# Kernel optimization log

Hardware: AMD Instinct MI355X
Metric: run time of the kernel (lower is better)

## Reference

```python
import jax, jax.numpy as jnp
import numpy as np
from jax import lax

# SLAYER neuron / simulation constants (netParams)
THETA = 1.0      # spike threshold
TAU_SR = 4.0     # PSP (SRM) kernel time constant
TAU_REF = 1.0    # refractory kernel time constant
SCALE_REF = 2.0  # refractory scale (kernel amplitude = -scaleRef*theta)
TAU_RHO = 1.0    # surrogate-gradient width (used in bwd only)
SCALE_RHO = 1.0

B, F_IN, T = 8, 6300, 500  # 6300 = 50*63*2
HID, OUT = 32, 20


def _alpha_scan(x, d):
    """Causal conv with alpha kernel k*d**k along last (time) axis via 2-state recurrence.
    x: [..., T]. y[t] = sum_{j<=t} x[j]*(t-j)*d**(t-j)."""
    xt = jnp.moveaxis(x, -1, 0)  # [T, ...]
    zero = jnp.zeros_like(xt[0])

    def step(carry, xi):
        z, y = carry
        y_new = d * (y + z)       # y[t] = d*(y[t-1] + z[t-1])
        z_new = d * z + xi        # z[t] = d*z[t-1] + x[t]
        return (z_new, y_new), y_new

    _, ys = lax.scan(step, (zero, zero), xt)
    return jnp.moveaxis(ys, 0, -1)


def psp(x):
    """SLAYER psp: convolve spike train with SRM kernel eps(k) = (k/tauSr)*exp(1-k/tauSr)."""
    d = float(np.exp(-1.0 / TAU_SR))
    return jnp.float32(np.e / TAU_SR) * _alpha_scan(x, d)


def _spike_impl(p):
    """Iterative threshold + refractory. p: [..., T] membrane input (post-psp, post-dense).
    Refractory kernel: ref(k) = -scaleRef*theta*(k/tauRef)*exp(1-k/tauRef), realized by the
    same 2-state alpha recurrence driven by emitted spikes."""
    d = float(np.exp(-1.0 / TAU_REF))
    C = jnp.float32(-SCALE_REF * THETA * np.e / TAU_REF)
    pt = jnp.moveaxis(p, -1, 0)  # [T, ...]
    zero = jnp.zeros_like(pt[0])

    def step(carry, pi):
        z, y = carry
        y_new = d * (y + z)                 # alpha state from past spikes (lag>=1)
        u = pi + C * y_new                  # membrane potential incl. refractory
        s = (u >= THETA).astype(pi.dtype)   # hard threshold
        z_new = d * z + s
        return (z_new, y_new), s

    _, ss = lax.scan(step, (zero, zero), pt)
    return jnp.moveaxis(ss, 0, -1)


def spike(p):
    return _spike_impl(p)


def setup_inputs() -> dict:
    key = jax.random.key(0)
    k1, k2, k3 = jax.random.split(key, 3)
    downsampled = (jax.random.uniform(k1, (B, F_IN, T)) < 0.05).astype(jnp.float32)
    w1 = jax.random.normal(k2, (HID, F_IN), jnp.float32) * 0.05
    w2 = jax.random.normal(k3, (OUT, HID), jnp.float32) * 0.3
    return {"downsampled": downsampled, "w1": w1, "w2": w2}


def reference(downsampled, w1, w2):
    # spike_1 = spike(psp(downsampled))
    s1 = spike(psp(downsampled))
    # spike_2 = spike(fc1(psp(spike_1)))
    s2 = spike(jnp.einsum('of,bft->bot', w1, psp(s1)))
    # spike_3 = spike(fc2(psp(spike_2)))
    s3 = spike(jnp.einsum('of,bft->bot', w2, psp(s2)))
    return s3
```

## Files before the change

kernel.cpp:

```cpp
#include <hip/hip_runtime.h>
#include <stdint.h>

#define NB 8
#define F_IN 6300
#define NT 500
#define HID 32
#define NOUT 20
#define NW 99

#define D_SR   0.7788007830714049f
#define S_SR   0.6795704571147613f
#define D_REF  0.36787944117144233f
#define C_REF  -5.43656365691809f

__global__ __launch_bounds__(256) void k0_transpose(const float* __restrict__ w1,
                                                    float* __restrict__ w1t) {
  __shared__ float tl[64][33];
  const int f0 = blockIdx.x * 64;
  const int tid = threadIdx.x;
  const int r = tid & 63, g = tid >> 6;
#pragma unroll
  for (int oo = 0; oo < 32; oo += 4) {
    int o = oo + g;
    int f = f0 + r;
    tl[r][o] = (f < F_IN) ? w1[o * F_IN + f] : 0.f;
  }
  __syncthreads();
#pragma unroll
  for (int k = 0; k < 8; k++) {
    int idx = k * 256 + tid;
    int rr = idx >> 5, cc = idx & 31;
    int f = f0 + rr;
    if (f < F_IN) w1t[(size_t)f * 32 + cc] = tl[rr][cc];
  }
}

#define CH_T 100

__global__ __launch_bounds__(64, 1) void k1_layer1(const float* __restrict__ x,
                                                   uint64_t* __restrict__ masks) {
  __shared__ __align__(16) float tileT[64][104];
  const int wi = blockIdx.x;
  const int b  = blockIdx.y;
  const int lane = threadIdx.x;
  const int f = wi * 64 + lane;
  const uint64_t vmask = __ballot(f < F_IN);
  const float* xblk = x + (size_t)b * F_IN * NT;
  uint64_t* mrow = masks + ((size_t)b * NW + wi) * NT;

  int goff[25], doff[25];
#pragma unroll
  for (int k = 0; k < 25; k++) {
    int idx = k * 64 + lane;
    int fid = idx / 25;
    int j = idx - fid * 25;
    int rf = wi * 64 + fid;
    if (rf >= F_IN) rf = F_IN - 1;
    goff[k] = rf * NT + 4 * j;
    doff[k] = fid * 104 + 4 * j;
  }

  float z1 = 0.f, y1 = 0.f, zr = 0.f, yr = 0.f;
  float* tbase = &tileT[0][0];

#pragma unroll 1
  for (int c = 0; c < 5; c++) {
    const float* gb = xblk + c * CH_T;
    float4 ld[25];
#pragma unroll
    for (int k = 0; k < 25; k++) ld[k] = *(const float4*)(gb + goff[k]);
#pragma unroll
    for (int k = 0; k < 25; k++) *(float4*)(tbase + doff[k]) = ld[k];

    const float4* lrow = (const float4*)&tileT[lane][0];
    float4 rbuf[4];
#pragma unroll
    for (int i = 0; i < 4; i++) rbuf[i] = lrow[i];
    uint64_t keep0 = 0, keep1 = 0;
#pragma unroll
    for (int g = 0; g < 25; g++) {
      float4 xq = rbuf[g & 3];
      if (g + 4 < 25) rbuf[g & 3] = lrow[g + 4];
      float xs[4] = {xq.x, xq.y, xq.z, xq.w};
#pragma unroll
      for (int e = 0; e < 4; e++) {
        const int tc = g * 4 + e;
        float xi = xs[e];
        y1 = __fmul_rn(D_SR, __fadd_rn(y1, z1));
        z1 = __fadd_rn(__fmul_rn(D_SR, z1), xi);
        float p = __fmul_rn(S_SR, y1);
        yr = __fmul_rn(D_REF, __fadd_rn(yr, zr));
        float u = __fadd_rn(p, __fmul_rn(C_REF, yr));
        bool s = (u >= 1.0f);
        zr = __fadd_rn(__fmul_rn(D_REF, zr), s ? 1.0f : 0.0f);
        uint64_t m = __ballot(s);
        if (tc < 64) { if (lane == tc)      keep0 = m; }
        else         { if (lane == tc - 64) keep1 = m; }
      }
    }
    uint64_t* mp = mrow + c * CH_T;
    mp[lane] = keep0 & vmask;
    if (lane < CH_T - 64) mp[64 + lane] = keep1 & vmask;
  }
}

__global__ __launch_bounds__(512) void k2_fc1(const float* __restrict__ w1t,
                                              const uint64_t* __restrict__ masks,
                                              double* __restrict__ R) {
  __shared__ double part[8][32];
  const int tid = threadIdx.x;
  const int wv = tid >> 6;
  const int lane = tid & 63;
  const int half = lane >> 5;
  const int o = lane & 31;
  const int b = blockIdx.x;
  const int t = blockIdx.y * 4 + (wv & 3);
  const int seg = wv >> 2;
  const int wbeg = seg * 50, wend = seg ? NW : 50;
  const uint64_t* mbase = masks + (size_t)b * NW * NT + t;
  const char* wrow = (const char*)w1t + o * 4;
  double acc0 = 0.0, acc1 = 0.0, acc2 = 0.0, acc3 = 0.0;

  int wi = wbeg + half;
  uint64_t mcur = (wi < wend) ? mbase[(size_t)wi * NT] : 0;
  for (; wi < wend; wi += 2) {
    uint64_t mnext = (wi + 2 < wend) ? mbase[(size_t)(wi + 2) * NT] : 0;
    const uint32_t base0 = ((uint32_t)wi << 13);
    uint32_t w = (uint32_t)mcur;
    uint32_t boff = base0;
#pragma unroll
    for (int sub = 0; sub < 2; sub++) {
      while (w) {
        uint32_t i0 = __builtin_ctz(w);                 uint32_t w1_ = w & (w - 1);
        uint32_t i1 = w1_ ? __builtin_ctz(w1_) : 0u;    uint32_t w2_ = w1_ ? (w1_ & (w1_ - 1)) : 0u;
        uint32_t i2 = w2_ ? __builtin_ctz(w2_) : 0u;    uint32_t w3_ = w2_ ? (w2_ & (w2_ - 1)) : 0u;
        uint32_t i3 = w3_ ? __builtin_ctz(w3_) : 0u;    w = w3_ ? (w3_ & (w3_ - 1)) : 0u;
        float a0 = *(const float*)(wrow + boff + (i0 << 7));
        float a1 = *(const float*)(wrow + boff + (i1 << 7));
        float a2 = *(const float*)(wrow + boff + (i2 << 7));
        float a3 = *(const float*)(wrow + boff + (i3 << 7));
        a1 = w1_ ? a1 : 0.0f;
        a2 = w2_ ? a2 : 0.0f;
        a3 = w3_ ? a3 : 0.0f;
        acc0 += (double)a0;
        acc1 += (double)a1;
        acc2 += (double)a2;
        acc3 += (double)a3;
      }
      w = (uint32_t)(mcur >> 32);
      boff = base0 + (32u << 7);
    }
    mcur = mnext;
  }
  double acc = (acc0 + acc1) + (acc2 + acc3);
  int hi2 = __shfl_xor(__double2hiint(acc), 32);
  int lo2 = __shfl_xor(__double2loint(acc), 32);
  acc += __hiloint2double(hi2, lo2);
  if (half == 0) part[wv][o] = acc;
  __syncthreads();
  if (wv < 4 && half == 0) {
    double tot = part[wv][o] + part[wv + 4][o];
    R[((size_t)b * HID + o) * NT + t] = tot;
  }
}

#define SNN_FAST_STEP(rin, EMIT)                                                \
  {                                                                             \
    y2 = __builtin_fma(dsr, y2, w);                                   \
    z2 = __builtin_fma(dsr, z2, (rin));                               \
    w  = dsr * z2;                                                              \
    double p  = ssr * y2;                                                       \
    double u0 = __builtin_fma(cr, q, p);                                        \
    double u1 = u0 + K;                                                         \
    double u  = sp ? u1 : u0;                                                   \
    bool s = (u >= 1.0);                                                        \
    double yr = q + (sp ? dre : 0.0);                                 \
    double zr = zrd + (sp ? 1.0 : 0.0);                           \
    zrd = dre * zr;                                                             \
    q = __builtin_fma(dre, yr, dre * zrd);                             \
    sp = s;                                                                     \
    EMIT                                                                        \
  }

__global__ __launch_bounds__(64) void k3_spike2(const double* __restrict__ R,
                                                uint32_t* __restrict__ s2m) {
  const int blk = blockIdx.x;
  const int lane = threadIdx.x;
  const int half = lane >> 5;
  const int b = blk * 2 + half;
  const int h = lane & 31;
  const double2* r2 = (const double2*)(R + ((size_t)b * HID + h) * NT);
  uint32_t* m0 = s2m + (size_t)(blk * 2) * NT;
  uint32_t* m1 = s2m + (size_t)(blk * 2 + 1) * NT;

  const double dsr = (double)D_SR, ssr = (double)S_SR;
  const double dre = (double)D_REF, cr = (double)C_REF;
  const double K = cr * dre;
  double y2 = 0, z2 = 0, w = 0, q = 0, zrd = 0;
  bool sp = false;

  double2 bufa[8], bufb[8];
#pragma unroll
  for (int i = 0; i < 8; i++) { bufa[i] = r2[i * 2]; bufb[i] = r2[i * 2 + 1]; }

  for (int g8 = 0; g8 < 16; g8++) {
#pragma unroll
    for (int j = 0; j < 8; j++) {
      const int g = g8 * 8 + j;
      if (g >= 125) break;
      const int t = g * 4;
      double2 va = bufa[j], vb = bufb[j];
      SNN_FAST_STEP(va.x, { uint64_t m = __ballot(s);
        if (lane == 0) { m0[t] = (uint32_t)m; m1[t] = (uint32_t)(m >> 32); } })
      SNN_FAST_STEP(va.y, { uint64_t m = __ballot(s);
        if (lane == 0) { m0[t + 1] = (uint32_t)m; m1[t + 1] = (uint32_t)(m >> 32); } })
      SNN_FAST_STEP(vb.x, { uint64_t m = __ballot(s);
        if (lane == 0) { m0[t + 2] = (uint32_t)m; m1[t + 2] = (uint32_t)(m >> 32); } })
      SNN_FAST_STEP(vb.y, { uint64_t m = __ballot(s);
        if (lane == 0) { m0[t + 3] = (uint32_t)m; m1[t + 3] = (uint32_t)(m >> 32); } })
      if (g + 8 < 125) { bufa[j] = r2[(g + 8) * 2]; bufb[j] = r2[(g + 8) * 2 + 1]; }
    }
  }
}

__global__ __launch_bounds__(256) void k4_fc2(const float* __restrict__ w2,
                                              const uint32_t* __restrict__ s2m,
                                              double* __restrict__ R3) {
  __shared__ float w2l[NOUT * HID];
  const int tid = threadIdx.x;
  for (int i = tid; i < NOUT * HID; i += 256) w2l[i] = w2[i];
  __syncthreads();
  int id = blockIdx.x * 256 + tid;
  if (id >= NB * NOUT * NT) return;
  int t = id % NT;
  int bo = id / NT;
  int o = bo % NOUT;
  int b = bo / NOUT;
  uint32_t m = s2m[(size_t)b * NT + t];
  const float* wr = w2l + o * HID;
  double acc = 0.0;
  while (m) {
    uint32_t i0 = __builtin_ctz(m);                 uint32_t m1_ = m & (m - 1);
    uint32_t i1 = m1_ ? __builtin_ctz(m1_) : 0u;    uint32_t m2_ = m1_ ? (m1_ & (m1_ - 1)) : 0u;
    uint32_t i2 = m2_ ? __builtin_ctz(m2_) : 0u;    uint32_t m3_ = m2_ ? (m2_ & (m2_ - 1)) : 0u;
    uint32_t i3 = m3_ ? __builtin_ctz(m3_) : 0u;    m = m3_ ? (m3_ & (m3_ - 1)) : 0u;
    float a0 = wr[i0];
    float a1 = m1_ ? wr[i1] : 0.0f;
    float a2 = m2_ ? wr[i2] : 0.0f;
    float a3 = m3_ ? wr[i3] : 0.0f;
    acc += (double)a0;
    acc += (double)a1;
    acc += (double)a2;
    acc += (double)a3;
  }
  R3[id] = acc;
}

__global__ __launch_bounds__(64) void k5_out(const double* __restrict__ R3,
                                             float* __restrict__ out) {
  int id = blockIdx.x * 64 + threadIdx.x;
  if (id >= NB * NOUT) return;
  const double2* r2 = (const double2*)(R3 + (size_t)id * NT);
  float* orow = out + (size_t)id * NT;

  const double dsr = (double)D_SR, ssr = (double)S_SR;
  const double dre = (double)D_REF, cr = (double)C_REF;
  const double K = cr * dre;
  double y2 = 0, z2 = 0, w = 0, q = 0, zrd = 0;
  bool sp = false;

  double2 bufa[8], bufb[8];
#pragma unroll
  for (int i = 0; i < 8; i++) { bufa[i] = r2[i * 2]; bufb[i] = r2[i * 2 + 1]; }

  for (int g8 = 0; g8 < 16; g8++) {
#pragma unroll
    for (int j = 0; j < 8; j++) {
      const int g = g8 * 8 + j;
      if (g >= 125) break;
      double2 va = bufa[j], vb = bufb[j];
      float4 ov;
      SNN_FAST_STEP(va.x, { ov.x = s ? 1.0f : 0.0f; })
      SNN_FAST_STEP(va.y, { ov.y = s ? 1.0f : 0.0f; })
      SNN_FAST_STEP(vb.x, { ov.z = s ? 1.0f : 0.0f; })
      SNN_FAST_STEP(vb.y, { ov.w = s ? 1.0f : 0.0f; })
      *(float4*)(orow + g * 4) = ov;
      if (g + 8 < 125) { bufa[j] = r2[(g + 8) * 2]; bufb[j] = r2[(g + 8) * 2 + 1]; }
    }
  }
}

extern "C" void kernel_launch(void* const* d_in, const int* in_sizes, int n_in,
                              void* d_out, int out_size, void* d_ws, size_t ws_size,
                              hipStream_t stream) {
  const float* x  = (const float*)d_in[0];
  const float* w1 = (const float*)d_in[1];
  const float* w2 = (const float*)d_in[2];
  float* out = (float*)d_out;

  uint8_t* ws = (uint8_t*)d_ws;
  const size_t W1T_BYTES  = (size_t)F_IN * HID * 4;
  const size_t MASK_BYTES = (size_t)NB * NW * NT * 8;
  const size_t R_BYTES    = (size_t)NB * HID * NT * 8;
  const size_t S2M_BYTES  = (size_t)NB * NT * 4;
  float*    w1t   = (float*)ws;
  uint64_t* masks = (uint64_t*)(ws + W1T_BYTES);
  double*   R     = (double*)(ws + W1T_BYTES + MASK_BYTES);
  uint32_t* s2m   = (uint32_t*)(ws + W1T_BYTES + MASK_BYTES + R_BYTES);
  double*   R3    = (double*)(ws + W1T_BYTES + MASK_BYTES + R_BYTES + S2M_BYTES);

  k0_transpose<<<99, 256, 0, stream>>>(w1, w1t);
  k1_layer1<<<dim3(NW, NB), 64, 0, stream>>>(x, masks);
  k2_fc1<<<dim3(NB, NT / 4), 512, 0, stream>>>(w1t, masks, R);
  k3_spike2<<<4, 64, 0, stream>>>(R, s2m);
  k4_fc2<<<(NB * NOUT * NT + 255) / 256, 256, 0, stream>>>(w2, s2m, R3);
  k5_out<<<3, 64, 0, stream>>>(R3, out);
}
```

Baseline: 283.6 us.

## Pre-pack input spike trains into bitmasks in a wide parallel kernel

Adds a highly parallel pre-pass, merged with the weight transpose into one launch, that reads the float input spike trains and ballots them into 64-bit time masks per feature row. The layer-1 recurrence kernel then reads only eight words per feature instead of staging float tiles through shared memory. The goal is to move the bulk input read out of the low-occupancy serial scan kernel into a bandwidth-friendly kernel. The packing assumes inputs are exactly binary (it tests >0.5), and it adds a workspace buffer and one extra write and read of the packed data.

```diff
diff --git a/kernel.cpp b/kernel.cpp
--- a/kernel.cpp
+++ b/kernel.cpp
@@ -7,17 +7,41 @@
 #define HID 32
 #define NOUT 20
 #define NW 99
+#define NWD 8
 
 #define D_SR   0.7788007830714049f
 #define S_SR   0.6795704571147613f
 #define D_REF  0.36787944117144233f
 #define C_REF  -5.43656365691809f
 
-__global__ __launch_bounds__(256) void k0_transpose(const float* __restrict__ w1,
-                                                    float* __restrict__ w1t) {
+#define NROWB ((NB * F_IN) / 4)
+
+__global__ __launch_bounds__(256) void k0_pack(const float* __restrict__ x,
+                                               const float* __restrict__ w1,
+                                               uint64_t* __restrict__ xb,
+                                               float* __restrict__ w1t) {
+  const int bid = blockIdx.x;
+  const int tid = threadIdx.x;
+  if (bid < NROWB) {
+    const int row = bid * 4 + (tid >> 6);
+    const int lane = tid & 63;
+    const float* xr = x + (size_t)row * NT;
+    uint64_t m[8];
+#pragma unroll
+    for (int k = 0; k < 8; k++) {
+      int t = k * 64 + lane;
+      float v = (t < NT) ? xr[t] : 0.f;
+      m[k] = __ballot(v > 0.5f);
+    }
+    if (lane == 0) {
+      uint64_t* dst = xb + (size_t)row * NWD;
+#pragma unroll
+      for (int k = 0; k < 8; k++) dst[k] = m[k];
+    }
+    return;
+  }
   __shared__ float tl[64][33];
-  const int f0 = blockIdx.x * 64;
-  const int tid = threadIdx.x;
+  const int f0 = (bid - NROWB) * 64;
   const int r = tid & 63, g = tid >> 6;
 #pragma unroll
   for (int oo = 0; oo < 32; oo += 4) {
@@ -35,72 +59,47 @@
   }
 }
 
-#define CH_T 100
-
-__global__ __launch_bounds__(64, 1) void k1_layer1(const float* __restrict__ x,
+__global__ __launch_bounds__(64, 1) void k1_layer1(const uint64_t* __restrict__ xb,
                                                    uint64_t* __restrict__ masks) {
-  __shared__ __align__(16) float tileT[64][104];
   const int wi = blockIdx.x;
   const int b  = blockIdx.y;
   const int lane = threadIdx.x;
   const int f = wi * 64 + lane;
   const uint64_t vmask = __ballot(f < F_IN);
-  const float* xblk = x + (size_t)b * F_IN * NT;
+  const int fc = (f < F_IN) ? f : (F_IN - 1);
+  const uint64_t* xr = xb + ((size_t)b * F_IN + fc) * NWD;
   uint64_t* mrow = masks + ((size_t)b * NW + wi) * NT;
 
-  int goff[25], doff[25];
-#pragma unroll
-  for (int k = 0; k < 25; k++) {
-    int idx = k * 64 + lane;
-    int fid = idx / 25;
-    int j = idx - fid * 25;
-    int rf = wi * 64 + fid;
-    if (rf >= F_IN) rf = F_IN - 1;
-    goff[k] = rf * NT + 4 * j;
-    doff[k] = fid * 104 + 4 * j;
-  }
-
-  float z1 = 0.f, y1 = 0.f, zr = 0.f, yr = 0.f;
-  float* tbase = &tileT[0][0];
+  float y1 = 0.f, z1 = 0.f, yr = 0.f, zr = 0.f;
+  uint64_t wcur = xr[0];
 
 #pragma unroll 1
-  for (int c = 0; c < 5; c++) {
-    const float* gb = xblk + c * CH_T;
-    float4 ld[25];
-#pragma unroll
-    for (int k = 0; k < 25; k++) ld[k] = *(const float4*)(gb + goff[k]);
-#pragma unroll
-    for (int k = 0; k < 25; k++) *(float4*)(tbase + doff[k]) = ld[k];
-
-    const float4* lrow = (const float4*)&tileT[lane][0];
-    float4 rbuf[4];
-#pragma unroll
-    for (int i = 0; i < 4; i++) rbuf[i] = lrow[i];
-    uint64_t keep0 = 0, keep1 = 0;
-#pragma unroll
-    for (int g = 0; g < 25; g++) {
-      float4 xq = rbuf[g & 3];
-      if (g + 4 < 25) rbuf[g & 3] = lrow[g + 4];
-      float xs[4] = {xq.x, xq.y, xq.z, xq.w};
-#pragma unroll
-      for (int e = 0; e < 4; e++) {
-        const int tc = g * 4 + e;
-        float xi = xs[e];
-        y1 = __fmul_rn(D_SR, __fadd_rn(y1, z1));
-        z1 = __fadd_rn(__fmul_rn(D_SR, z1), xi);
-        float p = __fmul_rn(S_SR, y1);
-        yr = __fmul_rn(D_REF, __fadd_rn(yr, zr));
-        float u = __fadd_rn(p, __fmul_rn(C_REF, yr));
-        bool s = (u >= 1.0f);
-        zr = __fadd_rn(__fmul_rn(D_REF, zr), s ? 1.0f : 0.0f);
-        uint64_t m = __ballot(s);
-        if (tc < 64) { if (lane == tc)      keep0 = m; }
-        else         { if (lane == tc - 64) keep1 = m; }
-      }
-    }
-    uint64_t* mp = mrow + c * CH_T;
-    mp[lane] = keep0 & vmask;
-    if (lane < CH_T - 64) mp[64 + lane] = keep1 & vmask;
+  for (int gg = 0; gg < 8; gg++) {
+    const int gn = (gg < 7) ? gg + 1 : 7;
+    uint64_t wnxt = xr[gn];
+    const uint32_t wlo = (uint32_t)wcur;
+    const uint32_t whi = (uint32_t)(wcur >> 32);
+    uint64_t keep = 0;
+#pragma unroll
+    for (int j = 0; j < 64; j++) {
+      const uint32_t bw = (j < 32) ? wlo : whi;
+      const bool xbit = ((bw >> (j & 31)) & 1u) != 0u;
+      float zm = __fmul_rn(D_SR, z1);
+      y1 = __fmul_rn(D_SR, __fadd_rn(y1, z1));
+      z1 = xbit ? __fadd_rn(zm, 1.0f) : zm;
+      float p = __fmul_rn(S_SR, y1);
+      yr = __fmul_rn(D_REF, __fadd_rn(yr, zr));
+      float u = __fadd_rn(p, __fmul_rn(C_REF, yr));
+      bool s = (u >= 1.0f);
+      float zrm = __fmul_rn(D_REF, zr);
+      zr = s ? __fadd_rn(zrm, 1.0f) : zrm;
+      uint64_t mball = __ballot(s);
+      if (lane == j) keep = mball;
+    }
+    uint64_t* mp = mrow + gg * 64;
+    if (gg < 7)                 mp[lane] = keep & vmask;
+    else if (lane < NT - 7*64)  mp[lane] = keep & vmask;
+    wcur = wnxt;
   }
 }
 
@@ -300,17 +299,19 @@
 
   uint8_t* ws = (uint8_t*)d_ws;
   const size_t W1T_BYTES  = (size_t)F_IN * HID * 4;
+  const size_t XBF_BYTES  = (size_t)NB * F_IN * NWD * 8;
   const size_t MASK_BYTES = (size_t)NB * NW * NT * 8;
   const size_t R_BYTES    = (size_t)NB * HID * NT * 8;
   const size_t S2M_BYTES  = (size_t)NB * NT * 4;
   float*    w1t   = (float*)ws;
-  uint64_t* masks = (uint64_t*)(ws + W1T_BYTES);
-  double*   R     = (double*)(ws + W1T_BYTES + MASK_BYTES);
-  uint32_t* s2m   = (uint32_t*)(ws + W1T_BYTES + MASK_BYTES + R_BYTES);
-  double*   R3    = (double*)(ws + W1T_BYTES + MASK_BYTES + R_BYTES + S2M_BYTES);
-
-  k0_transpose<<<99, 256, 0, stream>>>(w1, w1t);
-  k1_layer1<<<dim3(NW, NB), 64, 0, stream>>>(x, masks);
+  uint64_t* xbF   = (uint64_t*)(ws + W1T_BYTES);
+  uint64_t* masks = (uint64_t*)(ws + W1T_BYTES + XBF_BYTES);
+  double*   R     = (double*)(ws + W1T_BYTES + XBF_BYTES + MASK_BYTES);
+  uint32_t* s2m   = (uint32_t*)(ws + W1T_BYTES + XBF_BYTES + MASK_BYTES + R_BYTES);
+  double*   R3    = (double*)(ws + W1T_BYTES + XBF_BYTES + MASK_BYTES + R_BYTES + S2M_BYTES);
+
+  k0_pack<<<NROWB + 99, 256, 0, stream>>>(x, w1, xbF, w1t);
+  k1_layer1<<<dim3(NW, NB), 64, 0, stream>>>(xbF, masks);
   k2_fc1<<<dim3(NB, NT / 4), 512, 0, stream>>>(w1t, masks, R);
   k3_spike2<<<4, 64, 0, stream>>>(R, s2m);
   k4_fc2<<<(NB * NOUT * NT + 255) / 256, 256, 0, stream>>>(w2, s2m, R3);
```

Result: slower. 304.5 us (+7.4%).
